# Performance work log

Hardware: AMD Instinct MI355X
Metric: run time of the kernel (lower is better)

The kernel has to match this reference:

```python
import jax, jax.numpy as jnp
import numpy as np

N_ATOMS = 2_000_000
N_MOL = 100_000
ATOMS_PER_MOL = 20
FEAT_DIM = 128
MAX_Z = 86


def setup_inputs() -> dict:
    key = jax.random.key(0)
    k_z, k_f, k_w, k_b = jax.random.split(key, 4)
    z = jax.random.randint(k_z, (N_ATOMS,), 1, MAX_Z)  # avoid padding_idx 0
    f = jax.random.normal(k_f, (N_ATOMS, FEAT_DIM), dtype=jnp.float32)
    num_atoms = jnp.full((N_MOL,), ATOMS_PER_MOL, dtype=jnp.int64)
    w_e = jax.random.normal(k_w, (FEAT_DIM, 1), dtype=jnp.float32) / np.sqrt(FEAT_DIM)
    z_bias = jax.random.normal(k_b, (MAX_Z, 1), dtype=jnp.float32)
    z_bias = z_bias.at[0].set(0.0)  # padding_idx=0 row is zero
    return {"z": z, "f": f, "num_atoms": num_atoms, "w_e": w_e, "z_bias": z_bias}


def reference(z, f, num_atoms, w_e, z_bias):
    n_total = f.shape[0]
    n_mol = num_atoms.shape[0]
    # atomwise energy: linear(feat->1, no bias) + per-element embedding bias
    atomwise = f @ w_e + z_bias[z]  # [N, 1]
    # segment ids: molecule index for each atom (scatter_mol's index tensor)
    seg = jnp.repeat(jnp.arange(n_mol), num_atoms, total_repeat_length=n_total)
    e_total = jax.ops.segment_sum(atomwise, seg, num_segments=n_mol)  # [B, 1]
    return e_total
```

## Files before the change

### kernel.cpp

```cpp
#include <hip/hip_runtime.h>


#define FEAT 128
#define SCAN_CHUNK 1024
#define SCAN_THREADS 256

__global__ void k_partial_sums(const int* __restrict__ cnt, int n,
                               int* __restrict__ block_sums) {
    __shared__ int sdata[SCAN_THREADS];
    const int chunk_base = blockIdx.x * SCAN_CHUNK;
    int local = 0;
    for (int i = threadIdx.x; i < SCAN_CHUNK; i += SCAN_THREADS) {
        int idx = chunk_base + i;
        if (idx < n) local += cnt[idx];
    }
    sdata[threadIdx.x] = local;
    __syncthreads();
    for (int s = SCAN_THREADS / 2; s > 0; s >>= 1) {
        if (threadIdx.x < s) sdata[threadIdx.x] += sdata[threadIdx.x + s];
        __syncthreads();
    }
    if (threadIdx.x == 0) block_sums[blockIdx.x] = sdata[0];
}

__global__ void k_scan_block_sums(int* __restrict__ block_sums, int nb) {
    if (blockIdx.x == 0 && threadIdx.x == 0) {
        int acc = 0;
        for (int i = 0; i < nb; ++i) {
            int v = block_sums[i];
            block_sums[i] = acc;
            acc += v;
        }
    }
}

__global__ void k_offsets(const int* __restrict__ cnt, int n,
                          const int* __restrict__ block_sums,
                          int* __restrict__ offsets) {
    __shared__ int tsum[SCAN_THREADS];
    const int chunk_base = blockIdx.x * SCAN_CHUNK;
    const int t = threadIdx.x;
    const int per_thread = SCAN_CHUNK / SCAN_THREADS;
    const int base_idx = chunk_base + t * per_thread;

    int v[per_thread];
    int s = 0;
#pragma unroll
    for (int j = 0; j < per_thread; ++j) {
        int idx = base_idx + j;
        v[j] = (idx < n) ? cnt[idx] : 0;
        s += v[j];
    }
    tsum[t] = s;
    __syncthreads();

    for (int off = 1; off < SCAN_THREADS; off <<= 1) {
        int val = (t >= off) ? tsum[t - off] : 0;
        __syncthreads();
        tsum[t] += val;
        __syncthreads();
    }
    int running = block_sums[blockIdx.x] + (tsum[t] - s);
#pragma unroll
    for (int j = 0; j < per_thread; ++j) {
        int idx = base_idx + j;
        if (idx < n) offsets[idx] = running;
        running += v[j];
    }
}

__global__ void __launch_bounds__(256)
k_readout(const float* __restrict__ f, const int* __restrict__ z,
          const int* __restrict__ cnt, const int* __restrict__ offsets,
          const float* __restrict__ w_e, const float* __restrict__ z_bias,
          float* __restrict__ out, int n_mol) {
    const int lane = threadIdx.x & 63;
    const int wave = threadIdx.x >> 6;
    const int m = blockIdx.x * (blockDim.x >> 6) + wave;
    if (m >= n_mol) return;

    const int start = offsets[m];
    const int c = cnt[m];

    const int half = lane >> 5;
    const int qlane = lane & 31;

    const float4 w = reinterpret_cast<const float4*>(w_e)[qlane];

    float acc = 0.f;

    for (int i = lane; i < c; i += 64) acc += z_bias[z[start + i]];

    const float4* __restrict__ f4 = reinterpret_cast<const float4*>(f);
    const int pairs = c >> 1;
    for (int p = 0; p < pairs; ++p) {
        const size_t row = (size_t)(start + 2 * p + half);
        float4 fv = f4[row * (FEAT / 4) + qlane];
        acc = fmaf(fv.x, w.x, acc);
        acc = fmaf(fv.y, w.y, acc);
        acc = fmaf(fv.z, w.z, acc);
        acc = fmaf(fv.w, w.w, acc);
    }
    if (c & 1) {
        if (half == 0) {
            const size_t row = (size_t)(start + c - 1);
            float4 fv = f4[row * (FEAT / 4) + qlane];
            acc = fmaf(fv.x, w.x, acc);
            acc = fmaf(fv.y, w.y, acc);
            acc = fmaf(fv.z, w.z, acc);
            acc = fmaf(fv.w, w.w, acc);
        }
    }

#pragma unroll
    for (int off = 32; off > 0; off >>= 1) acc += __shfl_down(acc, off);
    if (lane == 0) out[m] = acc;
}

extern "C" void kernel_launch(void* const* d_in, const int* in_sizes, int n_in,
                              void* d_out, int out_size, void* d_ws, size_t ws_size,
                              hipStream_t stream) {
    const int*   z      = (const int*)d_in[0];
    const float* f      = (const float*)d_in[1];
    const int*   cnt    = (const int*)d_in[2];
    const float* w_e    = (const float*)d_in[3];
    const float* z_bias = (const float*)d_in[4];
    float* out = (float*)d_out;

    const int n_mol = in_sizes[2];

    int* offsets    = (int*)d_ws;
    const int nb    = (n_mol + SCAN_CHUNK - 1) / SCAN_CHUNK;
    int* block_sums = offsets + n_mol;

    k_partial_sums<<<nb, SCAN_THREADS, 0, stream>>>(cnt, n_mol, block_sums);
    k_scan_block_sums<<<1, 64, 0, stream>>>(block_sums, nb);
    k_offsets<<<nb, SCAN_THREADS, 0, stream>>>(cnt, n_mol, block_sums, offsets);

    const int waves_per_block = 4;
    const int grid = (n_mol + waves_per_block - 1) / waves_per_block;
    k_readout<<<grid, 256, 0, stream>>>(f, z, cnt, offsets, w_e, z_bias,
                                        out, n_mol);
}
```

Before: 193.9 us.

## Fold block-sum scan into offsets kernel and stage per-block outputs as float4

Removes the serial single-thread block-sum scan launch. Each offsets block now reduces the block sums of the chunks before it in parallel, which drops one kernel launch and the single-thread serial pass. The readout kernel also collects its four per-wave results in shared memory and writes them with one float4 store. That adds a block barrier and redundant prefix reads across blocks.

```diff
diff --git a/kernel.cpp b/kernel.cpp
--- a/kernel.cpp
+++ b/kernel.cpp
@@ -23,23 +23,27 @@
     if (threadIdx.x == 0) block_sums[blockIdx.x] = sdata[0];
 }
 
-__global__ void k_scan_block_sums(int* __restrict__ block_sums, int nb) {
-    if (blockIdx.x == 0 && threadIdx.x == 0) {
-        int acc = 0;
-        for (int i = 0; i < nb; ++i) {
-            int v = block_sums[i];
-            block_sums[i] = acc;
-            acc += v;
-        }
-    }
-}
-
 __global__ void k_offsets(const int* __restrict__ cnt, int n,
                           const int* __restrict__ block_sums,
                           int* __restrict__ offsets) {
     __shared__ int tsum[SCAN_THREADS];
+    __shared__ int s_prefix;
+    const int t = threadIdx.x;
+
+    int p = 0;
+    for (int j = t; j < blockIdx.x; j += SCAN_THREADS) p += block_sums[j];
+    tsum[t] = p;
+    __syncthreads();
+    for (int s = SCAN_THREADS / 2; s > 0; s >>= 1) {
+        if (t < s) tsum[t] += tsum[t + s];
+        __syncthreads();
+    }
+    if (t == 0) s_prefix = tsum[0];
+    __syncthreads();
+    const int chunk_prefix = s_prefix;
+    __syncthreads();
+
     const int chunk_base = blockIdx.x * SCAN_CHUNK;
-    const int t = threadIdx.x;
     const int per_thread = SCAN_CHUNK / SCAN_THREADS;
     const int base_idx = chunk_base + t * per_thread;
 
@@ -60,7 +64,7 @@
         tsum[t] += val;
         __syncthreads();
     }
-    int running = block_sums[blockIdx.x] + (tsum[t] - s);
+    int running = chunk_prefix + (tsum[t] - s);
 #pragma unroll
     for (int j = 0; j < per_thread; ++j) {
         int idx = base_idx + j;
@@ -74,35 +78,35 @@
           const int* __restrict__ cnt, const int* __restrict__ offsets,
           const float* __restrict__ w_e, const float* __restrict__ z_bias,
           float* __restrict__ out, int n_mol) {
+    __shared__ float s_out[4];
     const int lane = threadIdx.x & 63;
     const int wave = threadIdx.x >> 6;
-    const int m = blockIdx.x * (blockDim.x >> 6) + wave;
-    if (m >= n_mol) return;
+    const int m = blockIdx.x * 4 + wave;
 
-    const int start = offsets[m];
-    const int c = cnt[m];
+    if (m < n_mol) {
+        const int start = offsets[m];
+        const int c = cnt[m];
 
-    const int half = lane >> 5;
-    const int qlane = lane & 31;
+        const int half = lane >> 5;
+        const int qlane = lane & 31;
 
-    const float4 w = reinterpret_cast<const float4*>(w_e)[qlane];
+        const float4 w = reinterpret_cast<const float4*>(w_e)[qlane];
 
-    float acc = 0.f;
+        float acc = 0.f;
 
-    for (int i = lane; i < c; i += 64) acc += z_bias[z[start + i]];
+        for (int i = lane; i < c; i += 64) acc += z_bias[z[start + i]];
 
-    const float4* __restrict__ f4 = reinterpret_cast<const float4*>(f);
-    const int pairs = c >> 1;
-    for (int p = 0; p < pairs; ++p) {
-        const size_t row = (size_t)(start + 2 * p + half);
-        float4 fv = f4[row * (FEAT / 4) + qlane];
-        acc = fmaf(fv.x, w.x, acc);
-        acc = fmaf(fv.y, w.y, acc);
-        acc = fmaf(fv.z, w.z, acc);
-        acc = fmaf(fv.w, w.w, acc);
-    }
-    if (c & 1) {
-        if (half == 0) {
+        const float4* __restrict__ f4 = reinterpret_cast<const float4*>(f);
+        const int pairs = c >> 1;
+        for (int p = 0; p < pairs; ++p) {
+            const size_t row = (size_t)(start + 2 * p + half);
+            float4 fv = f4[row * (FEAT / 4) + qlane];
+            acc = fmaf(fv.x, w.x, acc);
+            acc = fmaf(fv.y, w.y, acc);
+            acc = fmaf(fv.z, w.z, acc);
+            acc = fmaf(fv.w, w.w, acc);
+        }
+        if ((c & 1) && half == 0) {
             const size_t row = (size_t)(start + c - 1);
             float4 fv = f4[row * (FEAT / 4) + qlane];
             acc = fmaf(fv.x, w.x, acc);
@@ -110,11 +114,22 @@
             acc = fmaf(fv.z, w.z, acc);
             acc = fmaf(fv.w, w.w, acc);
         }
-    }
 
 #pragma unroll
-    for (int off = 32; off > 0; off >>= 1) acc += __shfl_down(acc, off);
-    if (lane == 0) out[m] = acc;
+        for (int off = 32; off > 0; off >>= 1) acc += __shfl_down(acc, off);
+        if (lane == 0) s_out[wave] = acc;
+    }
+    __syncthreads();
+
+    if (threadIdx.x == 0) {
+        const int base = blockIdx.x * 4;
+        if (base + 3 < n_mol) {
+            float4 v = make_float4(s_out[0], s_out[1], s_out[2], s_out[3]);
+            *reinterpret_cast<float4*>(out + base) = v;
+        } else {
+            for (int i = 0; base + i < n_mol; ++i) out[base + i] = s_out[i];
+        }
+    }
 }
 
 extern "C" void kernel_launch(void* const* d_in, const int* in_sizes, int n_in,
@@ -134,7 +149,6 @@
     int* block_sums = offsets + n_mol;
 
     k_partial_sums<<<nb, SCAN_THREADS, 0, stream>>>(cnt, n_mol, block_sums);
-    k_scan_block_sums<<<1, 64, 0, stream>>>(block_sums, nb);
     k_offsets<<<nb, SCAN_THREADS, 0, stream>>>(cnt, n_mol, block_sums, offsets);
 
     const int waves_per_block = 4;
```

Result: faster. 181.2 us (-6.5%).
